# Kernel tuning notes

Hardware: AMD Instinct MI355X
Metric: run time of the kernel (lower is better)

The kernel has to match this reference:

```python
import jax, jax.numpy as jnp
import numpy as np

N = 100000
D = 128
E = 1600000


def setup_inputs() -> dict:
    key = jax.random.key(0)
    k1, k2, k3, k4 = jax.random.split(key, 4)
    x = jax.random.normal(k1, (N, D), dtype=jnp.float32)
    edge_index = jax.random.randint(k2, (2, E), 0, N, dtype=jnp.int64)
    edge_weight = jax.random.uniform(k3, (E,), dtype=jnp.float32)
    x0 = jax.random.normal(k4, (N, D), dtype=jnp.float32)
    return {
        "t": jnp.zeros((), dtype=jnp.float32),
        "x": x,
        "edge_index": edge_index,
        "edge_weight": edge_weight,
        "x0": x0,
        "alpha_train": jnp.zeros((), dtype=jnp.float32),
        "beta_train": jnp.zeros((), dtype=jnp.float32),
        "source_train": jnp.zeros((), dtype=jnp.float32),
    }


def reference(t, x, edge_index, edge_weight, x0, alpha_train, beta_train, source_train):
    # sigmoid-gated diffusion/reaction coefficients
    alpha = jax.nn.sigmoid(alpha_train) * 0.1
    beta = jax.nn.sigmoid(beta_train) * 0.1
    # sparse A @ x: out[row] += w * x[col]  (torch_sparse.spmm convention)
    row, col = edge_index[0], edge_index[1]
    msgs = x[col] * edge_weight[:, None]            # [E, D]
    ax = jax.ops.segment_sum(msgs, row, num_segments=N)  # [N, D]
    diffusion = ax - x
    reaction = -(x - 1.0) * x
    f = alpha * diffusion + beta * reaction
    source_term = jnp.clip(source_train * x0, -1.0, 1.0)
    return f + source_term * 0.1
```

## Files before the change

kernel.cpp:

```cpp
#include <hip/hip_runtime.h>
#include <math.h>


#define D_FEAT 128
#define RPB 128
#define NB_MAX 800
#define SORT_CAP 2560
#define EPB_COUNT 8192
#define EPB_PLACE 8192

__device__ __forceinline__ float sigmoid_f(float v) {
    return 1.0f / (1.0f + __expf(-v));
}

__device__ __forceinline__ unsigned bf16rn(float f) {
    unsigned u = __float_as_uint(f);
    return (u + 0x7FFFu + ((u >> 16) & 1u)) >> 16;
}

__global__ void zero_kernel(int* __restrict__ p, int n) {
    int i = blockIdx.x * blockDim.x + threadIdx.x;
    if (i < n) p[i] = 0;
}

__global__ __launch_bounds__(256) void cvtcount_kernel(const float* __restrict__ x,
                                                       unsigned short* __restrict__ xb,
                                                       int n8,
                                                       const int* __restrict__ rows,
                                                       int* __restrict__ cnt,
                                                       int E, int NB) {
    __shared__ int hist[NB_MAX];
    int t = threadIdx.x;
    for (int i = t; i < NB; i += 256) hist[i] = 0;

    if (xb) {
        const float4* x4 = (const float4*)x;
        for (int i = blockIdx.x * 256 + t; i < n8; i += gridDim.x * 256) {
            float4 f0 = x4[(size_t)i * 2];
            float4 f1 = x4[(size_t)i * 2 + 1];
            uint4 o;
            o.x = bf16rn(f0.x) | (bf16rn(f0.y) << 16);
            o.y = bf16rn(f0.z) | (bf16rn(f0.w) << 16);
            o.z = bf16rn(f1.x) | (bf16rn(f1.y) << 16);
            o.w = bf16rn(f1.z) | (bf16rn(f1.w) << 16);
            ((uint4*)xb)[i] = o;
        }
    }
    __syncthreads();

    int nE4 = E >> 2;
    int base4 = blockIdx.x * (EPB_COUNT / 4);
#pragma unroll
    for (int k = 0; k < EPB_COUNT / 4 / 256; ++k) {
        int i4 = base4 + k * 256 + t;
        if (i4 < nE4) {
            int4 r = ((const int4*)rows)[i4];
            atomicAdd(&hist[r.x >> 7], 1);
            atomicAdd(&hist[r.y >> 7], 1);
            atomicAdd(&hist[r.z >> 7], 1);
            atomicAdd(&hist[r.w >> 7], 1);
        }
    }
    if (blockIdx.x == 0 && t < (E & 3))
        atomicAdd(&hist[rows[(nE4 << 2) + t] >> 7], 1);
    __syncthreads();
    for (int i = t; i < NB; i += 256) {
        int c = hist[i];
        if (c) atomicAdd(&cnt[i], c);
    }
}

__global__ void scan_kernel(const int* __restrict__ cnt, int* __restrict__ bstart,
                            int* __restrict__ gcur, int NB) {
    int lane = threadIdx.x;
    int carry = 0;
    for (int base = 0; base < NB; base += 64) {
        int idx = base + lane;
        int v = (idx < NB) ? cnt[idx] : 0;
        int incl = v;
#pragma unroll
        for (int d = 1; d < 64; d <<= 1) {
            int tt = __shfl_up(incl, d);
            if (lane >= d) incl += tt;
        }
        int tot = __shfl(incl, 63);
        int excl = incl - v + carry;
        if (idx < NB) { bstart[idx] = excl; gcur[idx] = excl; }
        carry += tot;
    }
    if (lane == 0) bstart[NB] = carry;
}

__global__ __launch_bounds__(256) void place_kernel(const int* __restrict__ rows,
                                                    const int* __restrict__ cols,
                                                    const float* __restrict__ w,
                                                    const float* __restrict__ alpha_p,
                                                    int* __restrict__ gcur,
                                                    int2* __restrict__ raw, int E, int NB) {
    __shared__ int hist[NB_MAX];
    __shared__ int basep[NB_MAX];
    const float alpha = sigmoid_f(alpha_p[0]) * 0.1f;
    int t = threadIdx.x;
    for (int i = t; i < NB; i += 256) hist[i] = 0;
    __syncthreads();

    int base = blockIdx.x * EPB_PLACE;
#pragma unroll
    for (int k = 0; k < EPB_PLACE / 256; ++k) {
        int e = base + k * 256 + t;
        if (e < E) atomicAdd(&hist[rows[e] >> 7], 1);
    }
    __syncthreads();
    for (int i = t; i < NB; i += 256) {
        basep[i] = atomicAdd(&gcur[i], hist[i]);
        hist[i] = 0;
    }
    __syncthreads();
#pragma unroll
    for (int k = 0; k < EPB_PLACE / 256; ++k) {
        int e = base + k * 256 + t;
        if (e >= E) continue;
        int r = rows[e];
        int bkt = r >> 7;
        int rl  = r & 127;
        int rank = atomicAdd(&hist[bkt], 1);
        raw[basep[bkt] + rank] = make_int2((rl << 17) | cols[e],
                                           __float_as_int(w[e] * alpha));
    }
}

__global__ __launch_bounds__(256) void sort_kernel(const int2* __restrict__ raw,
                                                   int2* __restrict__ srt,
                                                   const int* __restrict__ bstart,
                                                   int* __restrict__ off, int N, int NB) {
    __shared__ int2 sbuf[SORT_CAP];
    __shared__ int2 obuf[SORT_CAP];
    __shared__ int hist[RPB];
    __shared__ int scanb[RPB];
    __shared__ int cursor[RPB];
    int b = blockIdx.x;
    int t = threadIdx.x;
    int bs = bstart[b], be = bstart[b + 1];
    int cntb = be - bs;
    if (t < RPB) hist[t] = 0;
    __syncthreads();

    bool fast = (cntb <= SORT_CAP);
    if (fast) {
        for (int i = t; i < cntb; i += 256) {
            int2 v = raw[bs + i];
            sbuf[i] = v;
            atomicAdd(&hist[v.x >> 17], 1);
        }
    } else {
        for (int i = t; i < cntb; i += 256)
            atomicAdd(&hist[raw[bs + i].x >> 17], 1);
    }
    __syncthreads();

    int v = 0;
    if (t < RPB) { v = hist[t]; scanb[t] = v; }
    __syncthreads();
    for (int d = 1; d < RPB; d <<= 1) {
        int tv = (t >= d && t < RPB) ? scanb[t - d] : 0;
        __syncthreads();
        if (t < RPB) scanb[t] += tv;
        __syncthreads();
    }
    if (t < RPB) {
        int incl = scanb[t];
        int excl = incl - v;
        int row = b * RPB + t;
        if (row < N) off[row] = bs + incl;
        cursor[t] = fast ? excl : (bs + excl);
    }
    __syncthreads();

    if (fast) {
        for (int i = t; i < cntb; i += 256) {
            int2 r = sbuf[i];
            int rl = r.x >> 17;
            int pos = atomicAdd(&cursor[rl], 1);
            obuf[pos] = make_int2(r.x & 0x1FFFF, r.y);
        }
        __syncthreads();
        for (int i = t; i < cntb; i += 256)
            srt[bs + i] = obuf[i];
    } else {
        for (int i = t; i < cntb; i += 256) {
            int2 r = raw[bs + i];
            int rl = r.x >> 17;
            int pos = atomicAdd(&cursor[rl], 1);
            srt[pos] = make_int2(r.x & 0x1FFFF, r.y);
        }
    }
}

__global__ void gather_bf16_kernel(const float* __restrict__ x,
                                   const unsigned short* __restrict__ xb,
                                   const float* __restrict__ x0,
                                   const int* __restrict__ off,
                                   const int2* __restrict__ col_w,
                                   const float* __restrict__ alpha_p,
                                   const float* __restrict__ beta_p,
                                   const float* __restrict__ src_p,
                                   float* __restrict__ out, int N) {
    const float alpha = sigmoid_f(alpha_p[0]) * 0.1f;
    const float beta  = sigmoid_f(beta_p[0]) * 0.1f;
    const float src   = src_p[0];

    int gtid = blockIdx.x * blockDim.x + threadIdx.x;
    int row  = gtid >> 6;
    if (row >= N) return;
    int lane  = threadIdx.x & 63;
    int half  = lane >> 5;
    int flane = lane & 31;

    int start = (row == 0) ? 0 : off[row - 1];
    int end   = off[row];

    const uint2* xb2 = (const uint2*)xb;
    float4 a0 = make_float4(0.f, 0.f, 0.f, 0.f);
    float4 a1 = make_float4(0.f, 0.f, 0.f, 0.f);
    float4 a2 = make_float4(0.f, 0.f, 0.f, 0.f);
    float4 a3 = make_float4(0.f, 0.f, 0.f, 0.f);

#define BF16_FMA(ACC, V, W)                                                    \
    {                                                                          \
        float b0 = __uint_as_float((V).x << 16);                               \
        float b1 = __uint_as_float((V).x & 0xFFFF0000u);                       \
        float b2 = __uint_as_float((V).y << 16);                               \
        float b3 = __uint_as_float((V).y & 0xFFFF0000u);                       \
        ACC.x += (W) * b0; ACC.y += (W) * b1;                                  \
        ACC.z += (W) * b2; ACC.w += (W) * b3;                                  \
    }

    int j = start + half;
    for (; j + 6 < end; j += 8) {
        int2 cw0 = col_w[j];
        int2 cw1 = col_w[j + 2];
        int2 cw2 = col_w[j + 4];
        int2 cw3 = col_w[j + 6];
        uint2 v0 = xb2[(size_t)cw0.x * 32 + flane];
        uint2 v1 = xb2[(size_t)cw1.x * 32 + flane];
        uint2 v2 = xb2[(size_t)cw2.x * 32 + flane];
        uint2 v3 = xb2[(size_t)cw3.x * 32 + flane];
        float w0 = __int_as_float(cw0.y);
        float w1 = __int_as_float(cw1.y);
        float w2 = __int_as_float(cw2.y);
        float w3 = __int_as_float(cw3.y);
        BF16_FMA(a0, v0, w0);
        BF16_FMA(a1, v1, w1);
        BF16_FMA(a2, v2, w2);
        BF16_FMA(a3, v3, w3);
    }
    for (; j + 2 < end; j += 4) {
        int2 cw0 = col_w[j];
        int2 cw1 = col_w[j + 2];
        uint2 v0 = xb2[(size_t)cw0.x * 32 + flane];
        uint2 v1 = xb2[(size_t)cw1.x * 32 + flane];
        float w0 = __int_as_float(cw0.y);
        float w1 = __int_as_float(cw1.y);
        BF16_FMA(a0, v0, w0);
        BF16_FMA(a1, v1, w1);
    }
    if (j < end) {
        int2 cw = col_w[j];
        uint2 v = xb2[(size_t)cw.x * 32 + flane];
        float wv = __int_as_float(cw.y);
        BF16_FMA(a0, v, wv);
    }
#undef BF16_FMA

    float4 acc;
    acc.x = (a0.x + a1.x) + (a2.x + a3.x);
    acc.y = (a0.y + a1.y) + (a2.y + a3.y);
    acc.z = (a0.z + a1.z) + (a2.z + a3.z);
    acc.w = (a0.w + a1.w) + (a2.w + a3.w);

    acc.x += __shfl_xor(acc.x, 32);
    acc.y += __shfl_xor(acc.y, 32);
    acc.z += __shfl_xor(acc.z, 32);
    acc.w += __shfl_xor(acc.w, 32);

    if (half == 0) {
        long long base = (long long)row * 32 + flane;
        float4 xv = ((const float4*)x)[base];
        float4 x0v = make_float4(0.f, 0.f, 0.f, 0.f);
        if (src != 0.0f)
            x0v = ((const float4*)x0)[base];
        float xs[4]  = {xv.x, xv.y, xv.z, xv.w};
        float zs[4]  = {x0v.x, x0v.y, x0v.z, x0v.w};
        float as[4]  = {acc.x, acc.y, acc.z, acc.w};
        float os[4];
#pragma unroll
        for (int k = 0; k < 4; ++k) {
            float reaction = -(xs[k] - 1.0f) * xs[k];
            float st = fminf(fmaxf(src * zs[k], -1.0f), 1.0f);
            os[k] = as[k] - alpha * xs[k] + beta * reaction + st * 0.1f;
        }
        ((float4*)out)[base] = make_float4(os[0], os[1], os[2], os[3]);
    }
}

__global__ void gather_f32_kernel(const float* __restrict__ x,
                                  const float* __restrict__ x0,
                                  const int* __restrict__ off,
                                  const int2* __restrict__ col_w,
                                  const float* __restrict__ alpha_p,
                                  const float* __restrict__ beta_p,
                                  const float* __restrict__ src_p,
                                  float* __restrict__ out, int N) {
    const float alpha = sigmoid_f(alpha_p[0]) * 0.1f;
    const float beta  = sigmoid_f(beta_p[0]) * 0.1f;
    const float src   = src_p[0];

    int gtid = blockIdx.x * blockDim.x + threadIdx.x;
    int row  = gtid >> 6;
    if (row >= N) return;
    int lane  = threadIdx.x & 63;
    int half  = lane >> 5;
    int flane = lane & 31;

    int start = (row == 0) ? 0 : off[row - 1];
    int end   = off[row];

    const float4* x4 = (const float4*)x;
    float4 a0 = make_float4(0.f, 0.f, 0.f, 0.f);
    float4 a1 = make_float4(0.f, 0.f, 0.f, 0.f);

    int j = start + half;
    for (; j + 2 < end; j += 4) {
        int2 cw0 = col_w[j];
        int2 cw1 = col_w[j + 2];
        float4 v0 = x4[(long long)cw0.x * 32 + flane];
        float4 v1 = x4[(long long)cw1.x * 32 + flane];
        float w0 = __int_as_float(cw0.y);
        float w1 = __int_as_float(cw1.y);
        a0.x += w0 * v0.x; a0.y += w0 * v0.y; a0.z += w0 * v0.z; a0.w += w0 * v0.w;
        a1.x += w1 * v1.x; a1.y += w1 * v1.y; a1.z += w1 * v1.z; a1.w += w1 * v1.w;
    }
    if (j < end) {
        int2 cw = col_w[j];
        float4 v = x4[(long long)cw.x * 32 + flane];
        float wv = __int_as_float(cw.y);
        a0.x += wv * v.x; a0.y += wv * v.y; a0.z += wv * v.z; a0.w += wv * v.w;
    }
    float4 acc;
    acc.x = a0.x + a1.x; acc.y = a0.y + a1.y;
    acc.z = a0.z + a1.z; acc.w = a0.w + a1.w;

    acc.x += __shfl_xor(acc.x, 32);
    acc.y += __shfl_xor(acc.y, 32);
    acc.z += __shfl_xor(acc.z, 32);
    acc.w += __shfl_xor(acc.w, 32);

    if (half == 0) {
        long long base = (long long)row * 32 + flane;
        float4 xv  = x4[base];
        float4 x0v = make_float4(0.f, 0.f, 0.f, 0.f);
        if (src != 0.0f)
            x0v = ((const float4*)x0)[base];
        float xs[4]  = {xv.x, xv.y, xv.z, xv.w};
        float zs[4]  = {x0v.x, x0v.y, x0v.z, x0v.w};
        float as[4]  = {acc.x, acc.y, acc.z, acc.w};
        float os[4];
#pragma unroll
        for (int k = 0; k < 4; ++k) {
            float reaction = -(xs[k] - 1.0f) * xs[k];
            float st = fminf(fmaxf(src * zs[k], -1.0f), 1.0f);
            os[k] = as[k] - alpha * xs[k] + beta * reaction + st * 0.1f;
        }
        ((float4*)out)[base] = make_float4(os[0], os[1], os[2], os[3]);
    }
}

extern "C" void kernel_launch(void* const* d_in, const int* in_sizes, int n_in,
                              void* d_out, int out_size, void* d_ws, size_t ws_size,
                              hipStream_t stream) {
    const float* x   = (const float*)d_in[1];
    const int*   ei  = (const int*)d_in[2];
    const float* ew  = (const float*)d_in[3];
    const float* x0  = (const float*)d_in[4];
    const float* alp = (const float*)d_in[5];
    const float* bet = (const float*)d_in[6];
    const float* src = (const float*)d_in[7];
    float* out = (float*)d_out;

    const int E = in_sizes[3];
    const int N = out_size / D_FEAT;
    const int* rows = ei;
    const int* cols = ei + E;

    const int NB = (N + RPB - 1) / RPB;
    const int nCntBlk = (E + EPB_COUNT - 1) / EPB_COUNT;
    const int nPlcBlk = (E + EPB_PLACE - 1) / EPB_PLACE;

    char* ws = (char*)d_ws;
    char* ws_end = (char*)d_ws + ws_size;
    int* cnt    = (int*)ws;  ws += ((size_t)NB * 4 + 15) & ~15ull;
    int* bstart = (int*)ws;  ws += ((size_t)(NB + 1) * 4 + 15) & ~15ull;
    int* gcur   = (int*)ws;  ws += ((size_t)NB * 4 + 15) & ~15ull;
    int* off    = (int*)ws;  ws += ((size_t)N * 4 + 15) & ~15ull;
    int2* col_w = (int2*)ws; ws += ((size_t)E * 8 + 15) & ~15ull;

    int2* raw;
    if ((size_t)out_size >= (size_t)E * 8) {
        raw = (int2*)d_out;
    } else {
        raw = (int2*)ws;     ws += ((size_t)E * 8 + 15) & ~15ull;
    }

    unsigned short* xb = nullptr;
    size_t xb_bytes = ((size_t)N * D_FEAT * 2 + 15) & ~15ull;
    if (ws + xb_bytes <= ws_end) {
        xb = (unsigned short*)ws;  ws += xb_bytes;
    }

    zero_kernel<<<(NB + 255) / 256, 256, 0, stream>>>(cnt, NB);
    {
        int n8 = (N * D_FEAT) / 8;
        cvtcount_kernel<<<nCntBlk, 256, 0, stream>>>(x, xb, n8, rows, cnt, E, NB);
    }
    scan_kernel<<<1, 64, 0, stream>>>(cnt, bstart, gcur, NB);
    place_kernel<<<nPlcBlk, 256, 0, stream>>>(rows, cols, ew, alp, gcur, raw, E, NB);
    sort_kernel<<<NB, 256, 0, stream>>>(raw, col_w, bstart, off, N, NB);
    {
        long long threads = (long long)N * 64;
        int grid = (int)((threads + 255) / 256);
        if (xb)
            gather_bf16_kernel<<<grid, 256, 0, stream>>>(x, xb, x0, off, col_w,
                                                         alp, bet, src, out, N);
        else
            gather_f32_kernel<<<grid, 256, 0, stream>>>(x, x0, off, col_w,
                                                        alp, bet, src, out, N);
    }
}
```

Baseline: 326.4 us.

## Replace global count/scan pre-pass with per-block local bucketing and directory merge

Removes the separate zero, histogram-count and scan kernels. Each place block now builds its own histogram, scans it locally, bucket-sorts its edges in shared memory, and writes them contiguously into an arena together with a per-block directory of bucket offsets and lengths. The sort kernel merges each bucket's segments from all blocks using a scan over the directory and a binary search per element. Bucket output positions come from an atomic cursor, so buckets are no longer in order, and the gather kernels read each bucket's start from a new bstart2 array. This cuts a full pass over the row indices and the scattered global writes, at the cost of extra shared memory, the directory traffic and binary-search work in sort.

```diff
diff --git a/kernel.cpp b/kernel.cpp
--- a/kernel.cpp
+++ b/kernel.cpp
@@ -6,8 +6,8 @@
 #define RPB 128
 #define NB_MAX 800
 #define SORT_CAP 2560
-#define EPB_COUNT 8192
-#define EPB_PLACE 8192
+#define EPB 8192
+#define MAXBLK 256
 
 __device__ __forceinline__ float sigmoid_f(float v) {
     return 1.0f / (1.0f + __expf(-v));
@@ -18,162 +18,175 @@
     return (u + 0x7FFFu + ((u >> 16) & 1u)) >> 16;
 }
 
-__global__ void zero_kernel(int* __restrict__ p, int n) {
-    int i = blockIdx.x * blockDim.x + threadIdx.x;
-    if (i < n) p[i] = 0;
-}
-
-__global__ __launch_bounds__(256) void cvtcount_kernel(const float* __restrict__ x,
-                                                       unsigned short* __restrict__ xb,
-                                                       int n8,
-                                                       const int* __restrict__ rows,
-                                                       int* __restrict__ cnt,
-                                                       int E, int NB) {
-    __shared__ int hist[NB_MAX];
-    int t = threadIdx.x;
-    for (int i = t; i < NB; i += 256) hist[i] = 0;
-
-    if (xb) {
-        const float4* x4 = (const float4*)x;
-        for (int i = blockIdx.x * 256 + t; i < n8; i += gridDim.x * 256) {
-            float4 f0 = x4[(size_t)i * 2];
-            float4 f1 = x4[(size_t)i * 2 + 1];
-            uint4 o;
-            o.x = bf16rn(f0.x) | (bf16rn(f0.y) << 16);
-            o.y = bf16rn(f0.z) | (bf16rn(f0.w) << 16);
-            o.z = bf16rn(f1.x) | (bf16rn(f1.y) << 16);
-            o.w = bf16rn(f1.z) | (bf16rn(f1.w) << 16);
-            ((uint4*)xb)[i] = o;
-        }
-    }
-    __syncthreads();
-
-    int nE4 = E >> 2;
-    int base4 = blockIdx.x * (EPB_COUNT / 4);
-#pragma unroll
-    for (int k = 0; k < EPB_COUNT / 4 / 256; ++k) {
-        int i4 = base4 + k * 256 + t;
-        if (i4 < nE4) {
-            int4 r = ((const int4*)rows)[i4];
-            atomicAdd(&hist[r.x >> 7], 1);
-            atomicAdd(&hist[r.y >> 7], 1);
-            atomicAdd(&hist[r.z >> 7], 1);
-            atomicAdd(&hist[r.w >> 7], 1);
-        }
-    }
-    if (blockIdx.x == 0 && t < (E & 3))
-        atomicAdd(&hist[rows[(nE4 << 2) + t] >> 7], 1);
-    __syncthreads();
-    for (int i = t; i < NB; i += 256) {
-        int c = hist[i];
-        if (c) atomicAdd(&cnt[i], c);
-    }
-}
-
-__global__ void scan_kernel(const int* __restrict__ cnt, int* __restrict__ bstart,
-                            int* __restrict__ gcur, int NB) {
-    int lane = threadIdx.x;
-    int carry = 0;
-    for (int base = 0; base < NB; base += 64) {
-        int idx = base + lane;
-        int v = (idx < NB) ? cnt[idx] : 0;
-        int incl = v;
-#pragma unroll
-        for (int d = 1; d < 64; d <<= 1) {
-            int tt = __shfl_up(incl, d);
-            if (lane >= d) incl += tt;
-        }
-        int tot = __shfl(incl, 63);
-        int excl = incl - v + carry;
-        if (idx < NB) { bstart[idx] = excl; gcur[idx] = excl; }
-        carry += tot;
-    }
-    if (lane == 0) bstart[NB] = carry;
+__global__ __launch_bounds__(256) void cvt_kernel(const float* __restrict__ x,
+                                                  unsigned short* __restrict__ xb,
+                                                  int n8, int* __restrict__ cursors) {
+    int i = blockIdx.x * 256 + threadIdx.x;
+    if (blockIdx.x == 0 && threadIdx.x == 0) { cursors[0] = 0; cursors[1] = 0; }
+    if (!xb || i >= n8) return;
+    const float4* x4 = (const float4*)x;
+    float4 f0 = x4[(size_t)i * 2];
+    float4 f1 = x4[(size_t)i * 2 + 1];
+    uint4 o;
+    o.x = bf16rn(f0.x) | (bf16rn(f0.y) << 16);
+    o.y = bf16rn(f0.z) | (bf16rn(f0.w) << 16);
+    o.z = bf16rn(f1.x) | (bf16rn(f1.y) << 16);
+    o.w = bf16rn(f1.z) | (bf16rn(f1.w) << 16);
+    ((uint4*)xb)[i] = o;
 }
 
 __global__ __launch_bounds__(256) void place_kernel(const int* __restrict__ rows,
                                                     const int* __restrict__ cols,
                                                     const float* __restrict__ w,
                                                     const float* __restrict__ alpha_p,
-                                                    int* __restrict__ gcur,
-                                                    int2* __restrict__ raw, int E, int NB) {
+                                                    int* __restrict__ arenaCur,
+                                                    int2* __restrict__ arena,
+                                                    unsigned* __restrict__ dir,
+                                                    int* __restrict__ blkBase,
+                                                    int E, int NB) {
+    __shared__ int2 sbuf[EPB];
     __shared__ int hist[NB_MAX];
-    __shared__ int basep[NB_MAX];
-    const float alpha = sigmoid_f(alpha_p[0]) * 0.1f;
+    __shared__ int lexcl[NB_MAX];
+    __shared__ int scanb[256];
+    __shared__ int gbase_sh;
     int t = threadIdx.x;
+    int blk = blockIdx.x;
+    int base = blk * EPB;
     for (int i = t; i < NB; i += 256) hist[i] = 0;
     __syncthreads();
 
-    int base = blockIdx.x * EPB_PLACE;
-#pragma unroll
-    for (int k = 0; k < EPB_PLACE / 256; ++k) {
+#pragma unroll
+    for (int k = 0; k < EPB / 256; ++k) {
         int e = base + k * 256 + t;
         if (e < E) atomicAdd(&hist[rows[e] >> 7], 1);
     }
     __syncthreads();
-    for (int i = t; i < NB; i += 256) {
-        basep[i] = atomicAdd(&gcur[i], hist[i]);
-        hist[i] = 0;
-    }
-    __syncthreads();
-#pragma unroll
-    for (int k = 0; k < EPB_PLACE / 256; ++k) {
+
+    const int CHK = 4;
+    int loc[CHK];
+    int run = 0;
+#pragma unroll
+    for (int k = 0; k < CHK; ++k) {
+        int idx = t * CHK + k;
+        int v = (idx < NB) ? hist[idx] : 0;
+        loc[k] = run; run += v;
+    }
+    scanb[t] = run;
+    __syncthreads();
+    for (int d = 1; d < 256; d <<= 1) {
+        int tv = (t >= d) ? scanb[t - d] : 0;
+        __syncthreads();
+        scanb[t] += tv;
+        __syncthreads();
+    }
+    int excl = scanb[t] - run;
+    int total = scanb[255];
+#pragma unroll
+    for (int k = 0; k < CHK; ++k) {
+        int idx = t * CHK + k;
+        if (idx < NB) lexcl[idx] = excl + loc[k];
+    }
+    if (t == 0) gbase_sh = atomicAdd(arenaCur, total);
+    __syncthreads();
+    for (int i = t; i < NB; i += 256) hist[i] = lexcl[i];
+    __syncthreads();
+    int gbase = gbase_sh;
+    const float alpha = sigmoid_f(alpha_p[0]) * 0.1f;
+
+#pragma unroll
+    for (int k = 0; k < EPB / 256; ++k) {
         int e = base + k * 256 + t;
         if (e >= E) continue;
         int r = rows[e];
         int bkt = r >> 7;
         int rl  = r & 127;
-        int rank = atomicAdd(&hist[bkt], 1);
-        raw[basep[bkt] + rank] = make_int2((rl << 17) | cols[e],
-                                           __float_as_int(w[e] * alpha));
-    }
-}
-
-__global__ __launch_bounds__(256) void sort_kernel(const int2* __restrict__ raw,
-                                                   int2* __restrict__ srt,
-                                                   const int* __restrict__ bstart,
-                                                   int* __restrict__ off, int N, int NB) {
+        int pos = atomicAdd(&hist[bkt], 1);
+        sbuf[pos] = make_int2((rl << 17) | cols[e], __float_as_int(w[e] * alpha));
+    }
+    __syncthreads();
+
+    for (int i = t; i < total; i += 256) arena[gbase + i] = sbuf[i];
+    for (int b = t; b < NB; b += 256) {
+        int le  = lexcl[b];
+        int len = ((b + 1 < NB) ? lexcl[b + 1] : total) - le;
+        dir[(size_t)blk * NB + b] = ((unsigned)le << 14) | (unsigned)len;
+    }
+    if (t == 0) blkBase[blk] = gbase;
+}
+
+__global__ __launch_bounds__(256) void sort_kernel(const int2* __restrict__ arena,
+                                                   const unsigned* __restrict__ dir,
+                                                   const int* __restrict__ blkBase,
+                                                   int nBlk,
+                                                   int2* __restrict__ col_w,
+                                                   int* __restrict__ outCur,
+                                                   int* __restrict__ off,
+                                                   int* __restrict__ bstart2,
+                                                   int N, int NB) {
     __shared__ int2 sbuf[SORT_CAP];
     __shared__ int2 obuf[SORT_CAP];
+    __shared__ int pre[MAXBLK + 1];
+    __shared__ int abase[MAXBLK];
+    __shared__ int scanb[256];
     __shared__ int hist[RPB];
-    __shared__ int scanb[RPB];
+    __shared__ int hscan[RPB];
     __shared__ int cursor[RPB];
+    __shared__ int gb_sh;
     int b = blockIdx.x;
     int t = threadIdx.x;
-    int bs = bstart[b], be = bstart[b + 1];
-    int cntb = be - bs;
+
+    int len = 0;
+    if (t < nBlk) {
+        unsigned d = dir[(size_t)t * NB + b];
+        len = (int)(d & 0x3FFFu);
+        abase[t] = blkBase[t] + (int)(d >> 14);
+    }
+    scanb[t] = len;
+    __syncthreads();
+    for (int d = 1; d < 256; d <<= 1) {
+        int tv = (t >= d) ? scanb[t - d] : 0;
+        __syncthreads();
+        scanb[t] += tv;
+        __syncthreads();
+    }
+    if (t < nBlk) pre[t] = scanb[t] - len;
+    if (t == 0) {
+        int total = scanb[nBlk - 1];
+        pre[nBlk] = total;
+        gb_sh = atomicAdd(outCur, total);
+    }
     if (t < RPB) hist[t] = 0;
     __syncthreads();
-
+    int cntb  = pre[nBlk];
+    int gbase = gb_sh;
     bool fast = (cntb <= SORT_CAP);
-    if (fast) {
-        for (int i = t; i < cntb; i += 256) {
-            int2 v = raw[bs + i];
-            sbuf[i] = v;
-            atomicAdd(&hist[v.x >> 17], 1);
-        }
-    } else {
-        for (int i = t; i < cntb; i += 256)
-            atomicAdd(&hist[raw[bs + i].x >> 17], 1);
+
+    for (int i = t; i < cntb; i += 256) {
+        int lo = 0, hi = nBlk;
+        while (hi - lo > 1) { int m = (lo + hi) >> 1; if (pre[m] <= i) lo = m; else hi = m; }
+        int2 rec = arena[abase[lo] + (i - pre[lo])];
+        if (fast) sbuf[i] = rec;
+        atomicAdd(&hist[rec.x >> 17], 1);
     }
     __syncthreads();
 
     int v = 0;
-    if (t < RPB) { v = hist[t]; scanb[t] = v; }
+    if (t < RPB) { v = hist[t]; hscan[t] = v; }
     __syncthreads();
     for (int d = 1; d < RPB; d <<= 1) {
-        int tv = (t >= d && t < RPB) ? scanb[t - d] : 0;
-        __syncthreads();
-        if (t < RPB) scanb[t] += tv;
+        int tv = (t >= d && t < RPB) ? hscan[t - d] : 0;
+        __syncthreads();
+        if (t < RPB) hscan[t] += tv;
         __syncthreads();
     }
     if (t < RPB) {
-        int incl = scanb[t];
+        int incl = hscan[t];
         int excl = incl - v;
         int row = b * RPB + t;
-        if (row < N) off[row] = bs + incl;
-        cursor[t] = fast ? excl : (bs + excl);
-    }
+        if (row < N) off[row] = gbase + incl;
+        cursor[t] = fast ? excl : (gbase + excl);
+    }
+    if (t == 0) bstart2[b] = gbase;
     __syncthreads();
 
     if (fast) {
@@ -185,13 +198,15 @@
         }
         __syncthreads();
         for (int i = t; i < cntb; i += 256)
-            srt[bs + i] = obuf[i];
+            col_w[gbase + i] = obuf[i];
     } else {
         for (int i = t; i < cntb; i += 256) {
-            int2 r = raw[bs + i];
+            int lo = 0, hi = nBlk;
+            while (hi - lo > 1) { int m = (lo + hi) >> 1; if (pre[m] <= i) lo = m; else hi = m; }
+            int2 r = arena[abase[lo] + (i - pre[lo])];
             int rl = r.x >> 17;
             int pos = atomicAdd(&cursor[rl], 1);
-            srt[pos] = make_int2(r.x & 0x1FFFF, r.y);
+            col_w[pos] = make_int2(r.x & 0x1FFFF, r.y);
         }
     }
 }
@@ -200,6 +215,7 @@
                                    const unsigned short* __restrict__ xb,
                                    const float* __restrict__ x0,
                                    const int* __restrict__ off,
+                                   const int* __restrict__ bstart2,
                                    const int2* __restrict__ col_w,
                                    const float* __restrict__ alpha_p,
                                    const float* __restrict__ beta_p,
@@ -216,7 +232,7 @@
     int half  = lane >> 5;
     int flane = lane & 31;
 
-    int start = (row == 0) ? 0 : off[row - 1];
+    int start = ((row & 127) == 0) ? bstart2[row >> 7] : off[row - 1];
     int end   = off[row];
 
     const uint2* xb2 = (const uint2*)xb;
@@ -306,6 +322,7 @@
 __global__ void gather_f32_kernel(const float* __restrict__ x,
                                   const float* __restrict__ x0,
                                   const int* __restrict__ off,
+                                  const int* __restrict__ bstart2,
                                   const int2* __restrict__ col_w,
                                   const float* __restrict__ alpha_p,
                                   const float* __restrict__ beta_p,
@@ -322,7 +339,7 @@
     int half  = lane >> 5;
     int flane = lane & 31;
 
-    int start = (row == 0) ? 0 : off[row - 1];
+    int start = ((row & 127) == 0) ? bstart2[row >> 7] : off[row - 1];
     int end   = off[row];
 
     const float4* x4 = (const float4*)x;
@@ -392,23 +409,26 @@
     const int* rows = ei;
     const int* cols = ei + E;
 
-    const int NB = (N + RPB - 1) / RPB;
-    const int nCntBlk = (E + EPB_COUNT - 1) / EPB_COUNT;
-    const int nPlcBlk = (E + EPB_PLACE - 1) / EPB_PLACE;
+    const int NB   = (N + RPB - 1) / RPB;
+    const int nBlk = (E + EPB - 1) / EPB;
 
     char* ws = (char*)d_ws;
     char* ws_end = (char*)d_ws + ws_size;
-    int* cnt    = (int*)ws;  ws += ((size_t)NB * 4 + 15) & ~15ull;
-    int* bstart = (int*)ws;  ws += ((size_t)(NB + 1) * 4 + 15) & ~15ull;
-    int* gcur   = (int*)ws;  ws += ((size_t)NB * 4 + 15) & ~15ull;
-    int* off    = (int*)ws;  ws += ((size_t)N * 4 + 15) & ~15ull;
-    int2* col_w = (int2*)ws; ws += ((size_t)E * 8 + 15) & ~15ull;
-
-    int2* raw;
-    if ((size_t)out_size >= (size_t)E * 8) {
-        raw = (int2*)d_out;
-    } else {
-        raw = (int2*)ws;     ws += ((size_t)E * 8 + 15) & ~15ull;
+    int*  off     = (int*)ws;  ws += ((size_t)N * 4 + 15) & ~15ull;
+    int*  bstart2 = (int*)ws;  ws += ((size_t)NB * 4 + 15) & ~15ull;
+    int2* col_w   = (int2*)ws; ws += ((size_t)E * 8 + 15) & ~15ull;
+
+    char* ob = (char*)d_out;
+    int2*     arena   = (int2*)ob;       ob += ((size_t)E * 8 + 15) & ~15ull;
+    unsigned* dir     = (unsigned*)ob;   ob += ((size_t)nBlk * NB * 4 + 15) & ~15ull;
+    int*      blkBase = (int*)ob;        ob += ((size_t)nBlk * 4 + 15) & ~15ull;
+    int*      cursors = (int*)ob;        ob += 16;
+    bool out_scratch_ok = (ob <= (char*)d_out + out_size);
+    if (!out_scratch_ok) {
+        arena   = (int2*)ws;     ws += ((size_t)E * 8 + 15) & ~15ull;
+        dir     = (unsigned*)ws; ws += ((size_t)nBlk * NB * 4 + 15) & ~15ull;
+        blkBase = (int*)ws;      ws += ((size_t)nBlk * 4 + 15) & ~15ull;
+        cursors = (int*)ws;      ws += 16;
     }
 
     unsigned short* xb = nullptr;
@@ -417,22 +437,23 @@
         xb = (unsigned short*)ws;  ws += xb_bytes;
     }
 
-    zero_kernel<<<(NB + 255) / 256, 256, 0, stream>>>(cnt, NB);
     {
         int n8 = (N * D_FEAT) / 8;
-        cvtcount_kernel<<<nCntBlk, 256, 0, stream>>>(x, xb, n8, rows, cnt, E, NB);
-    }
-    scan_kernel<<<1, 64, 0, stream>>>(cnt, bstart, gcur, NB);
-    place_kernel<<<nPlcBlk, 256, 0, stream>>>(rows, cols, ew, alp, gcur, raw, E, NB);
-    sort_kernel<<<NB, 256, 0, stream>>>(raw, col_w, bstart, off, N, NB);
+        int grid = xb ? (n8 + 255) / 256 : 1;
+        cvt_kernel<<<grid, 256, 0, stream>>>(x, xb, n8, cursors);
+    }
+    place_kernel<<<nBlk, 256, 0, stream>>>(rows, cols, ew, alp,
+                                           &cursors[0], arena, dir, blkBase, E, NB);
+    sort_kernel<<<NB, 256, 0, stream>>>(arena, dir, blkBase, nBlk,
+                                        col_w, &cursors[1], off, bstart2, N, NB);
     {
         long long threads = (long long)N * 64;
         int grid = (int)((threads + 255) / 256);
         if (xb)
-            gather_bf16_kernel<<<grid, 256, 0, stream>>>(x, xb, x0, off, col_w,
-                                                         alp, bet, src, out, N);
+            gather_bf16_kernel<<<grid, 256, 0, stream>>>(x, xb, x0, off, bstart2,
+                                                         col_w, alp, bet, src, out, N);
         else
-            gather_f32_kernel<<<grid, 256, 0, stream>>>(x, x0, off, col_w,
-                                                        alp, bet, src, out, N);
-    }
-}
+            gather_f32_kernel<<<grid, 256, 0, stream>>>(x, x0, off, bstart2,
+                                                        col_w, alp, bet, src, out, N);
+    }
+}
```

Result: faster. 315.2 us (-3.4%).
